# Kernel tuning notes

Measured on AMD Instinct MI355X. Metric: run time of the kernel, lower is better.

Reference implementation:

```python
import jax, jax.numpy as jnp
import numpy as np

N = 100000   # nodes
E = 640000   # edges
IN = 256     # raw input feature dim
D = 128      # post-MLP node feature dim (fixed in FilterGNN)


def setup_inputs() -> dict:
    key = jax.random.key(0)
    ks = jax.random.split(key, 10)
    x = jax.random.normal(ks[0], (N, IN), jnp.float32)
    alpha = jax.random.uniform(ks[1], (E, 1), jnp.float32)  # edge gate logits in [0,1)
    edge_index = jax.random.randint(ks[2], (2, E), 0, N, dtype=jnp.int32)
    norm = jnp.ones((E,), jnp.float32)  # passed to message in the original but unused
    # MLP `lin`: in_channels -> 512 -> 256 -> 128 (kaiming-normal weights, zero bias)
    def kaiming(k, fan_out, fan_in):
        return jax.random.normal(k, (fan_out, fan_in), jnp.float32) * jnp.sqrt(2.0 / fan_in)
    W1 = kaiming(ks[3], 512, IN); b1 = jnp.zeros((512,), jnp.float32)
    W2 = kaiming(ks[4], 256, 512); b2 = jnp.zeros((256,), jnp.float32)
    W3 = kaiming(ks[5], D, 256);  b3 = jnp.zeros((D,), jnp.float32)
    return {"x": x, "alpha": alpha, "edge_index": edge_index, "norm": norm,
            "W1": W1, "b1": b1, "W2": W2, "b2": b2, "W3": W3, "b3": b3}


def reference(x, alpha, edge_index, norm, W1, b1, W2, b2, W3, b3):
    # FilterGNN.lin: Linear-Tanh-Linear-Tanh-Linear  -> [N, 128]
    h = jnp.tanh(x @ W1.T + b1)
    h = jnp.tanh(h @ W2.T + b2)
    h = h @ W3.T + b3
    # FilterGraphConv1: gather x_j, elementwise relu gate, scatter-mean over targets.
    # (The [-1, H, C] view with H*C = 128 is a pure reshape; the gate broadcasts
    #  over all features, so the math is identical without the head split.)
    src, dst = edge_index[0], edge_index[1]
    gate = 2.0 * jax.nn.relu(jax.lax.stop_gradient(alpha) - 0.5)  # [E, 1]
    msg = h[src] * gate                                           # [E, 128] gather + gate
    sums = jax.ops.segment_sum(msg, dst, num_segments=N)          # [N, 128]
    cnt = jax.ops.segment_sum(jnp.ones((E,), h.dtype), dst, num_segments=N)
    out = sums / jnp.maximum(cnt, 1.0)[:, None]                   # scatter-mean (0 if no edges)
    return out
```

## Files before the change

kernel.cpp:

```cpp
#include <hip/hip_runtime.h>

typedef __attribute__((ext_vector_type(8))) short short8;
typedef __attribute__((ext_vector_type(4))) float f32x4;

__device__ __forceinline__ unsigned short f2bf(float f) {
    union { float f; unsigned u; } v; v.f = f;
    unsigned r = v.u + 0x7FFFu + ((v.u >> 16) & 1u);
    return (unsigned short)(r >> 16);
}
__device__ __forceinline__ float bf2f(unsigned short h) {
    union { unsigned u; float f; } v; v.u = ((unsigned)h) << 16;
    return v.f;
}

__device__ __forceinline__ float tanh_fast(float x) {
    float xc = fminf(fmaxf(x, -9.0f), 9.0f);
    float t  = __expf(2.0f * xc);
    return (t - 1.0f) * __builtin_amdgcn_rcpf(t + 1.0f);
}

__device__ __forceinline__ unsigned long long pack4(float4 v) {
    return (unsigned long long)f2bf(v.x)
         | ((unsigned long long)f2bf(v.y) << 16)
         | ((unsigned long long)f2bf(v.z) << 32)
         | ((unsigned long long)f2bf(v.w) << 48);
}

#define GLD16(gptr, lptr)                                                     \
    __builtin_amdgcn_global_load_lds(                                         \
        (const __attribute__((address_space(1))) unsigned int*)(gptr),        \
        (__attribute__((address_space(3))) unsigned int*)(lptr), 16, 0, 0)

__global__ __launch_bounds__(256) void cast_w(
    const float* __restrict__ W1, unsigned short* __restrict__ w1bf,
    const float* __restrict__ W2, unsigned short* __restrict__ w2bf,
    const float* __restrict__ W3, unsigned short* __restrict__ w3bf)
{
    int t = blockIdx.x * 256 + threadIdx.x;
    const float* s; unsigned short* d; int q;
    if (t < 32768)      { s = W1; d = w1bf; q = t; }
    else if (t < 65536) { s = W2; d = w2bf; q = t - 32768; }
    else if (t < 73728) { s = W3; d = w3bf; q = t - 65536; }
    else return;
    int base = q * 4;
    float4 v = *(const float4*)(s + base);
    *(unsigned long long*)(d + base) = pack4(v);
}

__global__ __launch_bounds__(256) void gemm1(
    const float* __restrict__ x, const unsigned short* __restrict__ W1,
    const float* __restrict__ b1, unsigned short* __restrict__ C, int M)
{
    __shared__ __align__(16) short lds[128 * 136];
    short* As = lds;
    short* Bs = lds + 128 * 64;

    const int tid  = threadIdx.x;
    const int wave = tid >> 6;
    const int lane = tid & 63;
    const int m0 = blockIdx.x * 128;
    const int n0 = blockIdx.y * 128;
    const int wm = (wave >> 1) * 64;
    const int wn = (wave & 1) * 64;
    const int lm = lane & 15;
    const int quad = lane >> 4;
    const int srow = lane >> 3;
    const int scol = ((lane & 7) ^ srow) * 8;
    const int cc0 = (quad ^ (lm & 7)) * 8;
    const int cc1 = ((4 + quad) ^ (lm & 7)) * 8;

    const int ac = tid & 7;
    const int arb = tid >> 3;

    f32x4 acc[4][4] = {};

    for (int kt = 0; kt < 4; ++kt) {
        const int k0 = kt * 64;
        #pragma unroll
        for (int j = 0; j < 4; ++j) {
            int r = arb + j * 32;
            int gr = m0 + r; if (gr >= M) gr = M - 1;
            const float* p = x + (size_t)gr * 256 + k0 + ac * 8;
            float4 a0 = *(const float4*)(p);
            float4 a1 = *(const float4*)(p + 4);
            unsigned long long* d =
                (unsigned long long*)&As[r * 64 + ((ac ^ (r & 7)) * 8)];
            d[0] = pack4(a0); d[1] = pack4(a1);
        }
        #pragma unroll
        for (int i = 0; i < 4; ++i) {
            int r0 = wave * 32 + i * 8;
            GLD16(W1 + (size_t)(n0 + r0 + srow) * 256 + k0 + scol, &Bs[r0 * 64]);
        }
        __syncthreads();
        #pragma unroll
        for (int ks = 0; ks < 2; ++ks) {
            const int cc = ks ? cc1 : cc0;
            short8 af[4], bf_[4];
            #pragma unroll
            for (int i = 0; i < 4; ++i) {
                af[i]  = *(const short8*)&As[(wm + i * 16 + lm) * 64 + cc];
                bf_[i] = *(const short8*)&Bs[(wn + i * 16 + lm) * 64 + cc];
            }
            #pragma unroll
            for (int im = 0; im < 4; ++im)
                #pragma unroll
                for (int in = 0; in < 4; ++in)
                    acc[im][in] = __builtin_amdgcn_mfma_f32_16x16x32_bf16(
                        af[im], bf_[in], acc[im][in], 0, 0, 0);
        }
        __syncthreads();
    }

    short* Ct = lds;
    #pragma unroll
    for (int in = 0; in < 4; ++in) {
        float bb = b1[n0 + wn + in * 16 + lm];
        int col = wn + in * 16 + lm;
        #pragma unroll
        for (int im = 0; im < 4; ++im) {
            #pragma unroll
            for (int r = 0; r < 4; ++r) {
                int row = wm + im * 16 + quad * 4 + r;
                Ct[row * 136 + col] = (short)f2bf(tanh_fast(acc[im][in][r] + bb));
            }
        }
    }
    __syncthreads();
    #pragma unroll
    for (int j = 0; j < 8; ++j) {
        int idx = j * 256 + tid;
        int row = idx >> 4, ch = idx & 15;
        int gm = m0 + row;
        if (gm < M) {
            uint4 v = *(const uint4*)&Ct[row * 136 + ch * 8];
            *(uint4*)(C + (size_t)gm * 512 + n0 + ch * 8) = v;
        }
    }
}

__global__ __launch_bounds__(256) void gemm23(
    const unsigned short* __restrict__ h1, const unsigned short* __restrict__ W2,
    const float* __restrict__ b2, const unsigned short* __restrict__ W3,
    const float* __restrict__ b3, unsigned short* __restrict__ hout, int M)
{
    __shared__ __align__(16) short As[64][64];
    __shared__ __align__(16) short Bs[256][64];
    __shared__ __align__(16) short h2s[64][264];

    const int tid  = threadIdx.x;
    const int wave = tid >> 6;
    const int lane = tid & 63;
    const int m0 = blockIdx.x * 64;
    const int wm = (wave >> 1) * 32;
    const int lm = lane & 15;
    const int quad = lane >> 4;
    const int srow = lane >> 3;
    const int scol = ((lane & 7) ^ srow) * 8;
    const int cc0 = (quad ^ (lm & 7)) * 8;
    const int cc1 = ((4 + quad) ^ (lm & 7)) * 8;

    {
        const int wn = (wave & 1) * 128;
        f32x4 acc[2][8] = {};
        for (int k0 = 0; k0 < 512; k0 += 64) {
            #pragma unroll
            for (int i = 0; i < 2; ++i) {
                int r0 = wave * 16 + i * 8;
                int gr = m0 + r0 + srow; if (gr >= M) gr = M - 1;
                GLD16(h1 + (size_t)gr * 512 + k0 + scol, &As[r0][0]);
            }
            #pragma unroll
            for (int i = 0; i < 8; ++i) {
                int r0 = wave * 64 + i * 8;
                GLD16(W2 + (size_t)(r0 + srow) * 512 + k0 + scol, &Bs[r0][0]);
            }
            __syncthreads();
            #pragma unroll
            for (int ks = 0; ks < 64; ks += 32) {
                const int cc = (ks == 0) ? cc0 : cc1;
                short8 af[2], bf_[8];
                #pragma unroll
                for (int i = 0; i < 2; ++i) af[i]  = *(const short8*)&As[wm + i * 16 + lm][cc];
                #pragma unroll
                for (int i = 0; i < 8; ++i) bf_[i] = *(const short8*)&Bs[wn + i * 16 + lm][cc];
                #pragma unroll
                for (int im = 0; im < 2; ++im)
                    #pragma unroll
                    for (int in = 0; in < 8; ++in)
                        acc[im][in] = __builtin_amdgcn_mfma_f32_16x16x32_bf16(
                            af[im], bf_[in], acc[im][in], 0, 0, 0);
            }
            __syncthreads();
        }
        #pragma unroll
        for (int im = 0; im < 2; ++im) {
            int rb = wm + im * 16 + quad * 4;
            #pragma unroll
            for (int in = 0; in < 8; ++in) {
                int col = wn + in * 16 + lm;
                float bv = b2[col];
                #pragma unroll
                for (int r = 0; r < 4; ++r)
                    h2s[rb + r][col] = (short)f2bf(tanh_fast(acc[im][in][r] + bv));
            }
        }
    }
    __syncthreads();

    {
        const int wn = (wave & 1) * 64;
        short (*Bs3)[64] = (short(*)[64])&Bs[0][0];
        f32x4 acc[2][4] = {};
        for (int k0 = 0; k0 < 256; k0 += 64) {
            #pragma unroll
            for (int i = 0; i < 4; ++i) {
                int r0 = wave * 32 + i * 8;
                GLD16(W3 + (size_t)(r0 + srow) * 256 + k0 + scol, &Bs3[r0][0]);
            }
            __syncthreads();
            #pragma unroll
            for (int ks = 0; ks < 64; ks += 32) {
                const int cc = (ks == 0) ? cc0 : cc1;
                short8 af[2], bf_[4];
                #pragma unroll
                for (int i = 0; i < 2; ++i)
                    af[i] = *(const short8*)&h2s[wm + i * 16 + lm][k0 + ks + quad * 8];
                #pragma unroll
                for (int i = 0; i < 4; ++i)
                    bf_[i] = *(const short8*)&Bs3[wn + i * 16 + lm][cc];
                #pragma unroll
                for (int im = 0; im < 2; ++im)
                    #pragma unroll
                    for (int in = 0; in < 4; ++in)
                        acc[im][in] = __builtin_amdgcn_mfma_f32_16x16x32_bf16(
                            af[im], bf_[in], acc[im][in], 0, 0, 0);
            }
            __syncthreads();
        }
        #pragma unroll
        for (int im = 0; im < 2; ++im) {
            int gm_base = m0 + wm + im * 16 + quad * 4;
            #pragma unroll
            for (int in = 0; in < 4; ++in) {
                int gn = wn + in * 16 + lm;
                float bv = b3[gn];
                #pragma unroll
                for (int r = 0; r < 4; ++r) {
                    int gm = gm_base + r;
                    if (gm < M)
                        hout[(size_t)gm * 128 + gn] = f2bf(acc[im][in][r] + bv);
                }
            }
        }
    }
}

__global__ __launch_bounds__(256) void edge_hist(
    const int* __restrict__ ei, const float* __restrict__ alpha,
    unsigned long long* __restrict__ deg, int E)
{
    int e = blockIdx.x * 256 + threadIdx.x;
    if (e >= E) return;
    int dst = ei[E + e];
    float gate = 2.0f * fmaxf(alpha[e] - 0.5f, 0.0f);
    atomicAdd(&deg[dst], 0x100000000ULL | (gate > 0.0f ? 1ULL : 0ULL));
}

__global__ __launch_bounds__(256) void scan1(
    const unsigned long long* __restrict__ deg, int* __restrict__ rowptr,
    int* __restrict__ cursor, int* __restrict__ partials, int N)
{
    __shared__ int sums[256];
    int base = blockIdx.x * 1024 + threadIdx.x * 4;
    int v[4];
    #pragma unroll
    for (int i = 0; i < 4; ++i) {
        int idx = base + i;
        v[i] = (idx < N) ? (int)(deg[idx] & 0xffffffffULL) : 0;
    }
    int s = v[0] + v[1] + v[2] + v[3];
    sums[threadIdx.x] = s;
    __syncthreads();
    for (int off = 1; off < 256; off <<= 1) {
        int t = (threadIdx.x >= off) ? sums[threadIdx.x - off] : 0;
        __syncthreads();
        sums[threadIdx.x] += t;
        __syncthreads();
    }
    int excl = sums[threadIdx.x] - s;
    if (threadIdx.x == 255) partials[blockIdx.x] = sums[255];
    int run = excl;
    #pragma unroll
    for (int i = 0; i < 4; ++i) {
        int idx = base + i;
        if (idx < N) { rowptr[idx] = run; cursor[idx] = run; }
        run += v[i];
    }
}

__global__ __launch_bounds__(256) void scan2(int* __restrict__ partials, int nb)
{
    __shared__ int s[256];
    int v = (threadIdx.x < nb) ? partials[threadIdx.x] : 0;
    s[threadIdx.x] = v;
    __syncthreads();
    for (int off = 1; off < 256; off <<= 1) {
        int t = (threadIdx.x >= off) ? s[threadIdx.x - off] : 0;
        __syncthreads();
        s[threadIdx.x] += t;
        __syncthreads();
    }
    partials[threadIdx.x] = s[threadIdx.x] - v;
}

__global__ __launch_bounds__(256) void edge_fill(
    const int* __restrict__ ei, const float* __restrict__ alpha,
    int* __restrict__ cursor, const int* __restrict__ partials,
    int2* __restrict__ recs, int E)
{
    int e = blockIdx.x * 256 + threadIdx.x;
    if (e >= E) return;
    float gate = 2.0f * fmaxf(alpha[e] - 0.5f, 0.0f);
    if (gate > 0.0f) {
        int dst = ei[E + e];
        int src = ei[e];
        int pos = atomicAdd(&cursor[dst], 1) + partials[dst >> 10];
        recs[pos] = make_int2(src, __float_as_int(gate));
    }
}

__global__ __launch_bounds__(256) void node_gather(
    const unsigned short* __restrict__ h, const unsigned long long* __restrict__ deg,
    const int* __restrict__ rowptr, const int* __restrict__ partials,
    const int2* __restrict__ recs, float* __restrict__ out, int N)
{
    int wave = threadIdx.x >> 6;
    int lane = threadIdx.x & 63;
    int node = blockIdx.x * 4 + wave;
    if (node >= N) return;
    unsigned long long d = deg[node];
    int dAll  = __builtin_amdgcn_readfirstlane((int)(d >> 32));
    int dG    = __builtin_amdgcn_readfirstlane((int)(d & 0xffffffffULL));
    int start = __builtin_amdgcn_readfirstlane(rowptr[node] + partials[node >> 10]);
    int qw = lane >> 4, ql = lane & 15;
    float a[8] = {};
    for (int j = 0; j < dG; j += 4) {
        int jj = j + qw;
        int idx = start + (jj < dG ? jj : dG - 1);
        int2 rec = recs[idx];
        float gate = (jj < dG) ? __int_as_float(rec.y) : 0.0f;
        uint4 u = *(const uint4*)(h + ((size_t)rec.x << 7) + ql * 8);
        a[0] += bf2f((unsigned short)(u.x & 0xffffu)) * gate;
        a[1] += bf2f((unsigned short)(u.x >> 16)) * gate;
        a[2] += bf2f((unsigned short)(u.y & 0xffffu)) * gate;
        a[3] += bf2f((unsigned short)(u.y >> 16)) * gate;
        a[4] += bf2f((unsigned short)(u.z & 0xffffu)) * gate;
        a[5] += bf2f((unsigned short)(u.z >> 16)) * gate;
        a[6] += bf2f((unsigned short)(u.w & 0xffffu)) * gate;
        a[7] += bf2f((unsigned short)(u.w >> 16)) * gate;
    }
    #pragma unroll
    for (int i = 0; i < 8; ++i) {
        a[i] += __shfl_xor(a[i], 16);
        a[i] += __shfl_xor(a[i], 32);
    }
    if (qw == 0) {
        float inv = 1.0f / fmaxf((float)dAll, 1.0f);
        float* op = out + ((size_t)node << 7) + ql * 8;
        *(float4*)(op)     = make_float4(a[0] * inv, a[1] * inv, a[2] * inv, a[3] * inv);
        *(float4*)(op + 4) = make_float4(a[4] * inv, a[5] * inv, a[6] * inv, a[7] * inv);
    }
}

extern "C" void kernel_launch(void* const* d_in, const int* in_sizes, int n_in,
                              void* d_out, int out_size, void* d_ws, size_t ws_size,
                              hipStream_t stream) {
    const float* x     = (const float*)d_in[0];
    const float* alpha = (const float*)d_in[1];
    const int*   ei    = (const int*)d_in[2];
    const float* W1 = (const float*)d_in[4];
    const float* b1 = (const float*)d_in[5];
    const float* W2 = (const float*)d_in[6];
    const float* b2 = (const float*)d_in[7];
    const float* W3 = (const float*)d_in[8];
    const float* b3 = (const float*)d_in[9];
    float* out = (float*)d_out;

    const int N = in_sizes[0] / 256;
    const int E = in_sizes[1];
    const int H1 = 512, D = 128;

    char* ws = (char*)d_ws;
    size_t off = 0;
    auto take = [&](size_t bytes) { char* p = ws + off; off = (off + bytes + 255) & ~(size_t)255; return p; };
    unsigned short* h1bf = (unsigned short*)take((size_t)N * H1 * 2);
    unsigned short* hbf  = (unsigned short*)take((size_t)N * D  * 2);
    unsigned short* w1bf = (unsigned short*)take((size_t)H1 * 256 * 2);
    unsigned short* w2bf = (unsigned short*)take((size_t)256 * H1 * 2);
    unsigned short* w3bf = (unsigned short*)take((size_t)D * 256 * 2);

    char* cbase = (char*)h1bf;
    size_t coff = 0;
    auto ctake = [&](size_t bytes) { char* p = cbase + coff; coff = (coff + bytes + 255) & ~(size_t)255; return p; };
    unsigned long long* deg = (unsigned long long*)ctake((size_t)N * 8);
    int*  rowptr   = (int*)ctake((size_t)N * 4);
    int*  cursor   = (int*)ctake((size_t)N * 4);
    int*  partials = (int*)ctake(256 * 4);
    int2* recs     = (int2*)ctake((size_t)E * 8);

    dim3 blk(256);

    cast_w<<<288, blk, 0, stream>>>(W1, w1bf, W2, w2bf, W3, w3bf);
    const int mblk = (N + 127) / 128;
    gemm1<<<dim3(mblk, 4), blk, 0, stream>>>(x, w1bf, b1, h1bf, N);
    gemm23<<<(N + 63) / 64, blk, 0, stream>>>(h1bf, w2bf, b2, w3bf, b3, hbf, N);

    hipMemsetAsync(deg, 0, (size_t)N * 8, stream);
    edge_hist<<<(E + 255) / 256, blk, 0, stream>>>(ei, alpha, deg, E);
    const int nb1 = (N + 1023) / 1024;
    scan1<<<nb1, blk, 0, stream>>>(deg, rowptr, cursor, partials, N);
    scan2<<<1, blk, 0, stream>>>(partials, nb1);
    edge_fill<<<(E + 255) / 256, blk, 0, stream>>>(ei, alpha, cursor, partials, recs, E);

    node_gather<<<(N + 3) / 4, blk, 0, stream>>>(hbf, deg, rowptr, partials, recs, out, N);
}
```

Measured before the change: 418.8 us.

## Stage full x row tile in LDS once and loop over all N-tiles in gemm1

gemm1 now loads each block's 128x256 slice of x into LDS once as bf16, then loops over the four 128-column output tiles, instead of launching four blocks per M-tile that each re-read and re-convert x. This cuts redundant global reads of the fp32 input. In exchange LDS use rises to about 80KB per block, which lowers occupancy, and the grid has a quarter as many blocks. The LDS-staged coalesced epilogue is replaced by direct scattered 2-byte global stores.

```diff
diff --git a/kernel.cpp b/kernel.cpp
--- a/kernel.cpp
+++ b/kernel.cpp
@@ -51,90 +51,75 @@
     const float* __restrict__ x, const unsigned short* __restrict__ W1,
     const float* __restrict__ b1, unsigned short* __restrict__ C, int M)
 {
-    __shared__ __align__(16) short lds[128 * 136];
-    short* As = lds;
-    short* Bs = lds + 128 * 64;
+    __shared__ __align__(16) short xs[128 * 256];
+    __shared__ __align__(16) short Bs[128 * 64];
 
     const int tid  = threadIdx.x;
     const int wave = tid >> 6;
     const int lane = tid & 63;
     const int m0 = blockIdx.x * 128;
-    const int n0 = blockIdx.y * 128;
     const int wm = (wave >> 1) * 64;
     const int wn = (wave & 1) * 64;
     const int lm = lane & 15;
     const int quad = lane >> 4;
     const int srow = lane >> 3;
     const int scol = ((lane & 7) ^ srow) * 8;
-    const int cc0 = (quad ^ (lm & 7)) * 8;
-    const int cc1 = ((4 + quad) ^ (lm & 7)) * 8;
-
-    const int ac = tid & 7;
-    const int arb = tid >> 3;
-
-    f32x4 acc[4][4] = {};
-
-    for (int kt = 0; kt < 4; ++kt) {
-        const int k0 = kt * 64;
+
+    #pragma unroll 4
+    for (int j = 0; j < 16; ++j) {
+        int idx = j * 256 + tid;
+        int r = idx >> 5, c = idx & 31;
+        int gr = m0 + r; if (gr >= M) gr = M - 1;
+        const float* p = x + (size_t)gr * 256 + c * 8;
+        float4 a0 = *(const float4*)(p);
+        float4 a1 = *(const float4*)(p + 4);
+        unsigned long long* d = (unsigned long long*)
+            &xs[r * 256 + (c >> 3) * 64 + (((c & 7) ^ (r & 7)) * 8)];
+        d[0] = pack4(a0); d[1] = pack4(a1);
+    }
+
+    for (int nh = 0; nh < 4; ++nh) {
+        const int n0 = nh * 128;
+        f32x4 acc[4][4] = {};
+        for (int kt = 0; kt < 4; ++kt) {
+            const int k0 = kt * 64;
+            #pragma unroll
+            for (int i = 0; i < 4; ++i) {
+                int r0 = wave * 32 + i * 8;
+                GLD16(W1 + (size_t)(n0 + r0 + srow) * 256 + k0 + scol, &Bs[r0 * 64]);
+            }
+            __syncthreads();
+            #pragma unroll
+            for (int ks = 0; ks < 2; ++ks) {
+                short8 af[4], bf_[4];
+                const int cc = (((ks * 4 + quad) ^ (lm & 7)) * 8);
+                #pragma unroll
+                for (int i = 0; i < 4; ++i) {
+                    af[i]  = *(const short8*)&xs[(wm + i * 16 + lm) * 256 + k0 + cc];
+                    bf_[i] = *(const short8*)&Bs[(wn + i * 16 + lm) * 64 + cc];
+                }
+                #pragma unroll
+                for (int im = 0; im < 4; ++im)
+                    #pragma unroll
+                    for (int in = 0; in < 4; ++in)
+                        acc[im][in] = __builtin_amdgcn_mfma_f32_16x16x32_bf16(
+                            af[im], bf_[in], acc[im][in], 0, 0, 0);
+            }
+            __syncthreads();
+        }
         #pragma unroll
-        for (int j = 0; j < 4; ++j) {
-            int r = arb + j * 32;
-            int gr = m0 + r; if (gr >= M) gr = M - 1;
-            const float* p = x + (size_t)gr * 256 + k0 + ac * 8;
-            float4 a0 = *(const float4*)(p);
-            float4 a1 = *(const float4*)(p + 4);
-            unsigned long long* d =
-                (unsigned long long*)&As[r * 64 + ((ac ^ (r & 7)) * 8)];
-            d[0] = pack4(a0); d[1] = pack4(a1);
-        }
-        #pragma unroll
-        for (int i = 0; i < 4; ++i) {
-            int r0 = wave * 32 + i * 8;
-            GLD16(W1 + (size_t)(n0 + r0 + srow) * 256 + k0 + scol, &Bs[r0 * 64]);
-        }
-        __syncthreads();
-        #pragma unroll
-        for (int ks = 0; ks < 2; ++ks) {
-            const int cc = ks ? cc1 : cc0;
-            short8 af[4], bf_[4];
-            #pragma unroll
-            for (int i = 0; i < 4; ++i) {
-                af[i]  = *(const short8*)&As[(wm + i * 16 + lm) * 64 + cc];
-                bf_[i] = *(const short8*)&Bs[(wn + i * 16 + lm) * 64 + cc];
-            }
-            #pragma unroll
-            for (int im = 0; im < 4; ++im)
-                #pragma unroll
-                for (int in = 0; in < 4; ++in)
-                    acc[im][in] = __builtin_amdgcn_mfma_f32_16x16x32_bf16(
-                        af[im], bf_[in], acc[im][in], 0, 0, 0);
-        }
-        __syncthreads();
-    }
-
-    short* Ct = lds;
-    #pragma unroll
-    for (int in = 0; in < 4; ++in) {
-        float bb = b1[n0 + wn + in * 16 + lm];
-        int col = wn + in * 16 + lm;
-        #pragma unroll
-        for (int im = 0; im < 4; ++im) {
-            #pragma unroll
-            for (int r = 0; r < 4; ++r) {
-                int row = wm + im * 16 + quad * 4 + r;
-                Ct[row * 136 + col] = (short)f2bf(tanh_fast(acc[im][in][r] + bb));
-            }
-        }
-    }
-    __syncthreads();
-    #pragma unroll
-    for (int j = 0; j < 8; ++j) {
-        int idx = j * 256 + tid;
-        int row = idx >> 4, ch = idx & 15;
-        int gm = m0 + row;
-        if (gm < M) {
-            uint4 v = *(const uint4*)&Ct[row * 136 + ch * 8];
-            *(uint4*)(C + (size_t)gm * 512 + n0 + ch * 8) = v;
+        for (int in = 0; in < 4; ++in) {
+            int gn = n0 + wn + in * 16 + lm;
+            float bb = b1[gn];
+            #pragma unroll
+            for (int im = 0; im < 4; ++im) {
+                #pragma unroll
+                for (int r = 0; r < 4; ++r) {
+                    int gm = m0 + wm + im * 16 + quad * 4 + r;
+                    if (gm < M)
+                        C[(size_t)gm * 512 + gn] = f2bf(tanh_fast(acc[im][in][r] + bb));
+                }
+            }
         }
     }
 }
@@ -413,7 +398,7 @@
 
     cast_w<<<288, blk, 0, stream>>>(W1, w1bf, W2, w2bf, W3, w3bf);
     const int mblk = (N + 127) / 128;
-    gemm1<<<dim3(mblk, 4), blk, 0, stream>>>(x, w1bf, b1, h1bf, N);
+    gemm1<<<dim3(mblk), blk, 0, stream>>>(x, w1bf, b1, h1bf, N);
     gemm23<<<(N + 63) / 64, blk, 0, stream>>>(h1bf, w2bf, b2, w3bf, b3, hbf, N);
 
     hipMemsetAsync(deg, 0, (size_t)N * 8, stream);
```

Result: slower. 446.4 us (+6.6%).
